# Kernel tuning notes

Hardware: AMD Instinct MI355X
Metric: run time of the kernel (lower is better)

The kernel has to match this reference:

```python
import jax, jax.numpy as jnp
import numpy as np
import math

T, B = 2048, 32
N_CLASSES = 64
D_MODEL = 512
N_LAYERS = 2
N_HEADS = 8
D_HEAD = 64
D_FF = N_HEADS * D_HEAD * 4  # 2048
E_VAL = (D_MODEL + 1) // 2   # 256 value-embedding dim
D_PE = D_MODEL // 2          # 256 positional dim (concatenated)
EPS_ATTN = 1e-6
EPS_LN = 1e-5


def _pe_table(t, d):
    pos = np.arange(t, dtype=np.float32)[:, None]
    div = np.exp(np.arange(0, d, 2, dtype=np.float32) * (-math.log(10000.0) / d))
    pe = np.zeros((t, d), dtype=np.float32)
    pe[:, 0::2] = np.sin(pos * div)
    pe[:, 1::2] = np.cos(pos * div)
    return jnp.asarray(pe)


def _ln(h, g, b):
    m = jnp.mean(h, axis=-1, keepdims=True)
    v = jnp.mean((h - m) ** 2, axis=-1, keepdims=True)
    return (h - m) * jax.lax.rsqrt(v + EPS_LN) * g + b


def setup_inputs() -> dict:
    key = jax.random.key(0)
    ks = jax.random.split(key, 12)
    s = 0.02
    L, dm, dff = N_LAYERS, D_MODEL, D_FF
    return {
        "x": jax.random.randint(ks[0], (T, B), 0, N_CLASSES),
        "E": jax.random.normal(ks[1], (N_CLASSES, E_VAL)) * s,
        "Wq": jax.random.normal(ks[2], (L, dm, dm)) * s, "bq": jnp.zeros((L, dm)),
        "Wk": jax.random.normal(ks[3], (L, dm, dm)) * s, "bk": jnp.zeros((L, dm)),
        "Wv": jax.random.normal(ks[4], (L, dm, dm)) * s, "bv": jnp.zeros((L, dm)),
        "Wo": jax.random.normal(ks[5], (L, dm, dm)) * s, "bo": jnp.zeros((L, dm)),
        "g1": jnp.ones((L, dm)), "be1": jnp.zeros((L, dm)),
        "W1": jax.random.normal(ks[6], (L, dm, dff)) * s, "b1": jnp.zeros((L, dff)),
        "W2": jax.random.normal(ks[7], (L, dff, dm)) * s, "b2": jnp.zeros((L, dm)),
        "g2": jnp.ones((L, dm)), "be2": jnp.zeros((L, dm)),
        "Wp": jax.random.normal(ks[8], (dm, N_CLASSES)) * s, "bp": jnp.zeros((N_CLASSES,)),
    }


def reference(x, E, Wq, bq, Wk, bk, Wv, bv, Wo, bo, g1, be1, W1, b1, W2, b2, g2, be2, Wp, bp):
    # embed tokens: x [T,B] -> [T,B,E_VAL]; concat positional (broadcast over batch) -> [T,B,D_MODEL]
    emb = E[x]
    pe = _pe_table(T, D_PE)
    h0 = jnp.concatenate([emb, jnp.broadcast_to(pe[:, None, :], (T, B, D_PE))], axis=-1)

    Si0 = jnp.zeros((N_LAYERS, B, N_HEADS, D_HEAD, D_HEAD), h0.dtype)  # sum_t k \otimes v
    Zi0 = jnp.zeros((N_LAYERS, B, N_HEADS, D_HEAD), h0.dtype)          # sum_t k

    phi = lambda u: jax.nn.elu(u) + 1.0  # linear-attention feature map

    def step(carry, xt):
        Si, Zi = carry
        h = xt  # [B, D_MODEL]
        for l in range(N_LAYERS):
            q = phi((h @ Wq[l] + bq[l]).reshape(B, N_HEADS, D_HEAD))
            k = phi((h @ Wk[l] + bk[l]).reshape(B, N_HEADS, D_HEAD))
            v = (h @ Wv[l] + bv[l]).reshape(B, N_HEADS, D_HEAD)
            Sl = Si[l] + k[..., :, None] * v[..., None, :]   # [B,H,D,D]
            Zl = Zi[l] + k
            num = jnp.einsum("bhd,bhdm->bhm", q, Sl)
            den = jnp.einsum("bhd,bhd->bh", q, Zl) + EPS_ATTN
            attn = (num / den[..., None]).reshape(B, N_HEADS * D_HEAD) @ Wo[l] + bo[l]
            h = _ln(h + attn, g1[l], be1[l])
            ff = jax.nn.relu(h @ W1[l] + b1[l]) @ W2[l] + b2[l]
            h = _ln(h + ff, g2[l], be2[l])
            Si = Si.at[l].set(Sl)
            Zi = Zi.at[l].set(Zl)
        return (Si, Zi), h

    _, ys = jax.lax.scan(step, (Si0, Zi0), h0)       # [T,B,D_MODEL]
    y_hat = jnp.transpose(ys, (1, 0, 2)) @ Wp + bp   # [B,T,N_CLASSES]
    return y_hat
```

## Files before the change

kernel.cpp:

```cpp
#include <hip/hip_runtime.h>


typedef unsigned short u16;
typedef __bf16 bf16x8 __attribute__((ext_vector_type(8)));
typedef float f32x4 __attribute__((ext_vector_type(4)));
typedef float f32x16 __attribute__((ext_vector_type(16)));

#define T_SEQ 2048
#define BATCH 32
#define NHEADS 8
#define CT 64
#define NCHUNK 32

#define SKEW(r, k) ((((k) + (((r) >> 3) << 3))) & 63)

__device__ __forceinline__ float b2f(u16 u) {
    union { unsigned int i; float f; } v; v.i = ((unsigned int)u) << 16; return v.f;
}
__device__ __forceinline__ u16 f2b(float f) {
    union { __bf16 b; u16 u; } v; v.b = (__bf16)f; return v.u;
}

__device__ __forceinline__ void gl_lds16(const u16* g, u16* l) {
    __builtin_amdgcn_global_load_lds(
        (const __attribute__((address_space(1))) void*)g,
        (__attribute__((address_space(3))) void*)l,
        16, 0, 0);
}

template<int ACT, bool RES>
__global__ __launch_bounds__(256) void gemm_mx(
    const u16* __restrict__ A, const u16* __restrict__ BT,
    const float* __restrict__ bias, const u16* __restrict__ R,
    u16* __restrict__ C,
    int M, int N, int K, int act_split, int nbn, int GM)
{
    __shared__ __align__(16) u16 As[128 * 64];
    __shared__ __align__(16) u16 Bs[128 * 64];

    const int bid = blockIdx.x;
    const int gsz = GM * nbn;
    const int grp = bid / gsz, rm = bid % gsz;
    const int bm = (grp * GM + rm % GM) * 128;
    const int bn = (rm / GM) * 128;

    const int tid = threadIdx.x;
    const int lane = tid & 63;
    const int w = tid >> 6;
    const int l32 = lane & 31;
    const int kh  = lane >> 5;
    const int wrow = (w >> 1) * 64, wcol = (w & 1) * 64;
    const int sr = lane >> 3;
    const int sg = lane & 7;

    f32x16 acc[2][2] = {};

    for (int k0 = 0; k0 < K; k0 += 64) {
        #pragma unroll
        for (int ch4 = 0; ch4 < 4; ch4++) {
            const int chunk = w * 4 + ch4;
            const int r = chunk * 8 + sr;
            const int gs = sg ^ (r & 7);
            gl_lds16(A  + (size_t)(bm + r) * K + k0 + gs * 8, As + chunk * 512);
            gl_lds16(BT + (size_t)(bn + r) * K + k0 + gs * 8, Bs + chunk * 512);
        }
        __syncthreads();
        #pragma unroll
        for (int step = 0; step < 4; step++) {
            const int gA = step * 2 + kh;
            bf16x8 af[2], bfv[2];
            #pragma unroll
            for (int i = 0; i < 2; i++) {
                const int r = wrow + i * 32 + l32;
                const int gq = gA ^ (r & 7);
                af[i] = *(const bf16x8*)&As[r * 64 + gq * 8];
            }
            #pragma unroll
            for (int j = 0; j < 2; j++) {
                const int r = wcol + j * 32 + l32;
                const int gq = gA ^ (r & 7);
                bfv[j] = *(const bf16x8*)&Bs[r * 64 + gq * 8];
            }
            #pragma unroll
            for (int i = 0; i < 2; i++)
                #pragma unroll
                for (int j = 0; j < 2; j++)
                    acc[i][j] = __builtin_amdgcn_mfma_f32_32x32x16_bf16(
                        af[i], bfv[j], acc[i][j], 0, 0, 0);
        }
        __syncthreads();
    }

    #pragma unroll
    for (int i = 0; i < 2; i++) {
        const int row0 = bm + wrow + i * 32 + 4 * kh;
        #pragma unroll
        for (int j = 0; j < 2; j++) {
            const int col = bn + wcol + j * 32 + l32;
            const float bb = bias[col];
            const bool phi = (ACT == 2) && (col < act_split);
            #pragma unroll
            for (int reg = 0; reg < 16; reg++) {
                const int m = row0 + (reg & 3) + 8 * (reg >> 2);
                float v = acc[i][j][reg] + bb;
                if (RES) v += b2f(R[(size_t)m * N + col]);
                if (ACT == 1) v = fmaxf(v, 0.f);
                if (ACT == 2) { if (phi) v = (v > 0.f) ? (v + 1.f) : __expf(v); }
                C[(size_t)m * N + col] = f2b(v);
            }
        }
    }
}

template<int BM, int BN, int WM, int WN>
__global__ __launch_bounds__(WM*WN*64) void gemm_sm(
    const u16* __restrict__ A, const u16* __restrict__ BT,
    const float* __restrict__ bias, float* __restrict__ C,
    int M, int N, int K)
{
    constexpr int BK = 32;
    constexpr int LDT = BK + 8;
    constexpr int NTHR = WM * WN * 64;
    __shared__ __align__(16) u16 As[BM * LDT];
    __shared__ __align__(16) u16 Bs[BN * LDT];

    const int tid = threadIdx.x;
    const int bm = blockIdx.y * BM;
    const int bn = blockIdx.x * BN;
    const int lane = tid & 63;
    const int wid = tid >> 6;
    const int wrow = (wid / WN) * (BM / WM);
    const int wcol = (wid % WN) * (BN / WN);
    constexpr int FM = BM / WM / 16;
    constexpr int FN = BN / WN / 16;
    const int lrow = lane & 15;
    const int lk = (lane >> 4) * 8;

    f32x4 acc[FM][FN] = {};

    for (int k0 = 0; k0 < K; k0 += BK) {
        #pragma unroll
        for (int g0 = 0; g0 < BM * 4; g0 += NTHR) {
            int g = g0 + tid;
            int row = g >> 2, kk = (g & 3) * 8;
            *(uint4*)&As[row * LDT + kk] =
                *(const uint4*)&A[(size_t)(bm + row) * K + k0 + kk];
        }
        #pragma unroll
        for (int g0 = 0; g0 < BN * 4; g0 += NTHR) {
            int g = g0 + tid;
            int row = g >> 2, kk = (g & 3) * 8;
            *(uint4*)&Bs[row * LDT + kk] =
                *(const uint4*)&BT[(size_t)(bn + row) * K + k0 + kk];
        }
        __syncthreads();
        bf16x8 af[FM], bfv[FN];
        #pragma unroll
        for (int i = 0; i < FM; i++)
            af[i] = *(const bf16x8*)&As[(wrow + i * 16 + lrow) * LDT + lk];
        #pragma unroll
        for (int j = 0; j < FN; j++)
            bfv[j] = *(const bf16x8*)&Bs[(wcol + j * 16 + lrow) * LDT + lk];
        #pragma unroll
        for (int i = 0; i < FM; i++)
            #pragma unroll
            for (int j = 0; j < FN; j++)
                acc[i][j] = __builtin_amdgcn_mfma_f32_16x16x32_bf16(
                    bfv[j], af[i], acc[i][j], 0, 0, 0);
        __syncthreads();
    }

    #pragma unroll
    for (int i = 0; i < FM; i++) {
        const int row = bm + wrow + i * 16 + lrow;
        #pragma unroll
        for (int j = 0; j < FN; j++) {
            const int col0 = bn + wcol + j * 16 + (lane >> 4) * 4;
            const float4 bb = *(const float4*)&bias[col0];
            float4 o = { acc[i][j][0] + bb.x, acc[i][j][1] + bb.y,
                         acc[i][j][2] + bb.z, acc[i][j][3] + bb.w };
            *(float4*)&C[(size_t)row * N + col0] = o;
        }
    }
}

__global__ __launch_bounds__(256) void prep_kernel(
    const float* __restrict__ Wq, const float* __restrict__ Wk,
    const float* __restrict__ Wv, const float* __restrict__ Wo,
    const float* __restrict__ W1, const float* __restrict__ W2,
    const float* __restrict__ Wp,
    const float* __restrict__ bq, const float* __restrict__ bk,
    const float* __restrict__ bv,
    u16* __restrict__ qkvT, u16* __restrict__ woT, u16* __restrict__ w1T,
    u16* __restrict__ w2T, u16* __restrict__ wpT, u16* __restrict__ pe,
    float* __restrict__ bqkv)
{
    __shared__ float tile[32][33];
    const int bid = blockIdx.x;
    const float* src; u16* dst; int K, N, bx, by;

    if (bid < 1536) {
        int l = bid / 768, r = bid % 768, m = r >> 8, t = r & 255;
        const float* s3[3] = { Wq, Wk, Wv };
        src = s3[m] + (size_t)l * 262144;
        dst = qkvT + (size_t)l * 786432 + (size_t)m * 262144;
        K = 512; N = 512; bx = t & 15; by = t >> 4;
    } else if (bid < 2048) {
        int r = bid - 1536, l = r >> 8, t = r & 255;
        src = Wo + (size_t)l * 262144; dst = woT + (size_t)l * 262144;
        K = 512; N = 512; bx = t & 15; by = t >> 4;
    } else if (bid < 4096) {
        int r = bid - 2048, l = r >> 10, t = r & 1023;
        src = W1 + (size_t)l * 1048576; dst = w1T + (size_t)l * 1048576;
        K = 512; N = 2048; bx = t & 63; by = t >> 6;
    } else if (bid < 6144) {
        int r = bid - 4096, l = r >> 10, t = r & 1023;
        src = W2 + (size_t)l * 1048576; dst = w2T + (size_t)l * 1048576;
        K = 2048; N = 512; bx = t & 15; by = t >> 4;
    } else if (bid < 6176) {
        int t = bid - 6144;
        src = Wp; dst = wpT; K = 512; N = 64; bx = t & 1; by = t >> 1;
    } else if (bid < 8224) {
        int id = (bid - 6176) * 256 + threadIdx.x;
        int t = id >> 8, j = id & 255;
        int i = j >> 1;
        float div = expf(-(float)(2 * i) * (9.210340371976184f / 256.f));
        float arg = (float)t * div;
        pe[id] = f2b((j & 1) ? cosf(arg) : sinf(arg));
        return;
    } else {
        int id = (bid - 8224) * 256 + threadIdx.x;
        if (id < 3072) {
            int l = id / 1536, i2 = id % 1536;
            float v = (i2 < 512) ? bq[l * 512 + i2]
                    : (i2 < 1024) ? bk[l * 512 + i2 - 512]
                                  : bv[l * 512 + i2 - 1024];
            bqkv[id] = v;
        }
        return;
    }

    int tx = threadIdx.x & 31, ty = threadIdx.x >> 5;
    #pragma unroll
    for (int yy = 0; yy < 4; yy++) {
        int k = by * 32 + ty + yy * 8;
        tile[ty + yy * 8][tx] = src[(size_t)k * N + bx * 32 + tx];
    }
    __syncthreads();
    #pragma unroll
    for (int yy = 0; yy < 4; yy++) {
        int n = bx * 32 + ty + yy * 8;
        dst[(size_t)n * K + by * 32 + tx] = f2b(tile[tx][ty + yy * 8]);
    }
}

__global__ __launch_bounds__(256) void embed_kernel(
    const int* __restrict__ x, const float* __restrict__ E,
    const u16* __restrict__ pe, u16* __restrict__ h, int b0)
{
    int idx = blockIdx.x * 256 + threadIdx.x;
    int e8 = idx * 8;
    int r = e8 >> 9;
    int c = e8 & 511;
    int t = r & (T_SEQ - 1);
    int b = b0 + (r >> 11);
    union { u16 u[8]; uint4 v; } o;
    if (c < 256) {
        const float* Ep = &E[(size_t)x[t * BATCH + b] * 256 + c];
        #pragma unroll
        for (int i = 0; i < 8; i++) o.u[i] = f2b(Ep[i]);
    } else {
        o.v = *(const uint4*)&pe[t * 256 + (c - 256)];
    }
    *(uint4*)&h[e8] = o.v;
}

__global__ __launch_bounds__(256) void attn_chunk_sums(
    const u16* __restrict__ qkv, u16* __restrict__ S, float* __restrict__ Z,
    int BHg)
{
    __shared__ __align__(16) u16 Kt[64 * 72], Vt[64 * 72];
    int bid = blockIdx.x;
    int bh = bid % BHg, c = bid / BHg;
    int bl = bh >> 3, hh = bh & 7;
    {
        const int m  = threadIdx.x & 7;
        const int d0 = m * 8;
        #pragma unroll
        for (int p = 0; p < 2; p++) {
            const int t = p * 32 + (threadIdx.x >> 3);
            size_t rr = ((size_t)(bl * T_SEQ + c * 64 + t)) * 1536 + hh * 64 + d0;
            uint4 kv = *(const uint4*)&qkv[rr + 512];
            uint4 vv = *(const uint4*)&qkv[rr + 1024];
            const u16* kp = (const u16*)&kv;
            const u16* vp = (const u16*)&vv;
            const int sk = (t + d0) & 63;
            u16* kb = &Kt[d0 * 72 + sk];
            u16* vb = &Vt[d0 * 72 + sk];
            #pragma unroll
            for (int s = 0; s < 8; s++) { kb[s * 72] = kp[s]; vb[s * 72] = vp[s]; }
        }
    }
    __syncthreads();
    int lane = threadIdx.x & 63;
    int w = threadIdx.x >> 6;
    int lrow = lane & 15, quad = lane >> 4;
    int m0 = w * 16;
    f32x4 acc[4] = {};
    #pragma unroll
    for (int k0 = 0; k0 < 64; k0 += 32) {
        const int ra = m0 + lrow;
        bf16x8 af = *(const bf16x8*)&Vt[ra * 72 + SKEW(ra, k0 + quad * 8)];
        #pragma unroll
        for (int jt = 0; jt < 4; jt++) {
            const int rb = jt * 16 + lrow;
            bf16x8 bf = *(const bf16x8*)&Kt[rb * 72 + SKEW(rb, k0 + quad * 8)];
            acc[jt] = __builtin_amdgcn_mfma_f32_16x16x32_bf16(bf, af, acc[jt], 0, 0, 0);
        }
    }
    size_t base = ((size_t)c * BHg + bh) * 4096;
    const int m = m0 + lrow;
    #pragma unroll
    for (int jt = 0; jt < 4; jt++) {
        const int d0 = jt * 16 + quad * 4;
        union { u16 q[4]; uint2 u; } pk;
        #pragma unroll
        for (int r = 0; r < 4; r++) pk.q[r] = f2b(acc[jt][r]);
        *(uint2*)&S[base + m * 64 + d0] = pk.u;
    }
    if (threadIdx.x < 64) {
        const int d = threadIdx.x;
        float z = 0.f;
        #pragma unroll
        for (int t8 = 0; t8 < 64; t8 += 8) {
            bf16x8 kk = *(const bf16x8*)&Kt[d * 72 + SKEW(d, t8)];
            #pragma unroll
            for (int u = 0; u < 8; u++) z += (float)kk[u];
        }
        Z[((size_t)c * BHg + bh) * 64 + d] = z;
    }
}

__global__ __launch_bounds__(256) void attn_prefix(
    u16* __restrict__ S, float* __restrict__ Z, int BHg)
{
    int gid = blockIdx.x * 256 + threadIdx.x;
    int bh = gid >> 12, e = gid & 4095;
    size_t stride = (size_t)BHg * 4096;
    size_t base = (size_t)bh * 4096 + e;
    float v[NCHUNK];
    #pragma unroll
    for (int c = 0; c < NCHUNK; c++) v[c] = b2f(S[base + c * stride]);
    float run = 0.f;
    #pragma unroll
    for (int c = 0; c < NCHUNK; c++) {
        float t = v[c]; S[base + c * stride] = f2b(run); run += t;
    }
    if (gid < BHg * 64) {
        size_t zb = (size_t)gid;
        size_t zs = (size_t)BHg * 64;
        float zv[NCHUNK];
        #pragma unroll
        for (int c = 0; c < NCHUNK; c++) zv[c] = Z[zb + c * zs];
        float zr = 0.f;
        #pragma unroll
        for (int c = 0; c < NCHUNK; c++) {
            float t = zv[c]; Z[zb + c * zs] = zr; zr += t;
        }
    }
}

__global__ __launch_bounds__(256) void attn_intra(
    const u16* __restrict__ qkv, const u16* __restrict__ Sp,
    const float* __restrict__ Zp, u16* __restrict__ out, int BHg)
{
    __shared__ __align__(16) u16 Qs[64 * 72], Ks[64 * 72], Vt[64 * 72],
                                 Ssh[64 * 72];
    __shared__ float Zsh[64], den2sh[64], den1sh[64];
    u16* Ps = Ks;
    int bid = blockIdx.x;
    int bh = bid % BHg, c = bid / BHg;
    int bl = bh >> 3, hh = bh & 7;
    size_t sbase = ((size_t)c * BHg + bh) * 4096;
    {
        const int m  = threadIdx.x & 7;
        const int d0 = m * 8;
        #pragma unroll
        for (int p = 0; p < 2; p++) {
            const int t = p * 32 + (threadIdx.x >> 3);
            size_t rr = ((size_t)(bl * T_SEQ + c * 64 + t)) * 1536 + hh * 64 + d0;
            *(uint4*)&Qs[t * 72 + d0]  = *(const uint4*)&qkv[rr];
            *(uint4*)&Ks[t * 72 + d0]  = *(const uint4*)&qkv[rr + 512];
            *(uint4*)&Ssh[t * 72 + d0] = *(const uint4*)&Sp[sbase + t * 64 + d0];
            uint4 vv = *(const uint4*)&qkv[rr + 1024];
            const u16* vp = (const u16*)&vv;
            const int sk = (t + d0) & 63;
            u16* vb = &Vt[d0 * 72 + sk];
            #pragma unroll
            for (int s = 0; s < 8; s++) vb[s * 72] = vp[s];
        }
    }
    if (threadIdx.x < 64)
        Zsh[threadIdx.x] = Zp[((size_t)c * BHg + bh) * 64 + threadIdx.x];
    __syncthreads();

    if (threadIdx.x < 64) {
        float s = 0.f;
        #pragma unroll
        for (int d8 = 0; d8 < 64; d8 += 8) {
            bf16x8 qq = *(const bf16x8*)&Qs[threadIdx.x * 72 + d8];
            #pragma unroll
            for (int u = 0; u < 8; u++) s += (float)qq[u] * Zsh[d8 + u];
        }
        den2sh[threadIdx.x] = s;
    }

    int lane = threadIdx.x & 63;
    int w = threadIdx.x >> 6;
    int lrow = lane & 15, quad = lane >> 4;
    int i0 = w * 16;

    f32x4 accp[4] = {};
    #pragma unroll
    for (int k0 = 0; k0 < 64; k0 += 32) {
        bf16x8 af = *(const bf16x8*)&Qs[(i0 + lrow) * 72 + k0 + quad * 8];
        #pragma unroll
        for (int jt = 0; jt < 4; jt++) {
            bf16x8 bf = *(const bf16x8*)&Ks[(jt * 16 + lrow) * 72 + k0 + quad * 8];
            accp[jt] = __builtin_amdgcn_mfma_f32_16x16x32_bf16(af, bf, accp[jt], 0, 0, 0);
        }
    }
    __syncthreads();
    #pragma unroll
    for (int r = 0; r < 4; r++) {
        int row = i0 + quad * 4 + r;
        float d1 = 0.f;
        #pragma unroll
        for (int jt = 0; jt < 4; jt++) {
            int col = jt * 16 + lrow;
            float pv = (col <= row) ? accp[jt][r] : 0.f;
            d1 += pv;
            Ps[row * 72 + col] = f2b(pv);
        }
        #pragma unroll
        for (int off = 1; off < 16; off <<= 1)
            d1 += __shfl_xor(d1, off, 64);
        if (lrow == 0) den1sh[row] = d1;
    }
    __syncthreads();

    f32x4 acco[4] = {};
    #pragma unroll
    for (int k0 = 0; k0 < 64; k0 += 32) {
        bf16x8 ps = *(const bf16x8*)&Ps[(i0 + lrow) * 72 + k0 + quad * 8];
        #pragma unroll
        for (int jt = 0; jt < 4; jt++) {
            const int rv = jt * 16 + lrow;
            bf16x8 vf = *(const bf16x8*)&Vt[rv * 72 + SKEW(rv, k0 + quad * 8)];
            acco[jt] = __builtin_amdgcn_mfma_f32_16x16x32_bf16(vf, ps, acco[jt], 0, 0, 0);
        }
    }
    #pragma unroll
    for (int k0 = 0; k0 < 64; k0 += 32) {
        bf16x8 qf = *(const bf16x8*)&Qs[(i0 + lrow) * 72 + k0 + quad * 8];
        #pragma unroll
        for (int jt = 0; jt < 4; jt++) {
            bf16x8 sf = *(const bf16x8*)&Ssh[(jt * 16 + lrow) * 72 + k0 + quad * 8];
            acco[jt] = __builtin_amdgcn_mfma_f32_16x16x32_bf16(sf, qf, acco[jt], 0, 0, 0);
        }
    }
    const int i = i0 + lrow;
    const float inv = 1.f / (den1sh[i] + den2sh[i] + 1e-6f);
    size_t orow = ((size_t)(bl * T_SEQ + c * 64 + i)) * 512 + hh * 64;
    #pragma unroll
    for (int jt = 0; jt < 4; jt++) {
        const int m0 = jt * 16 + quad * 4;
        union { u16 q[4]; uint2 u; } pk;
        #pragma unroll
        for (int r = 0; r < 4; r++) pk.q[r] = f2b(acco[jt][r] * inv);
        *(uint2*)&out[orow + m0] = pk.u;
    }
}

__global__ __launch_bounds__(256) void ln_kernel(
    const u16* __restrict__ s_in,
    const float* __restrict__ g, const float* __restrict__ be, u16* __restrict__ out)
{
    int row = blockIdx.x * 4 + (threadIdx.x >> 6);
    int lane = threadIdx.x & 63;
    size_t base = (size_t)row * 512 + lane * 8;
    uint4 hv = *(const uint4*)&s_in[base];
    const u16* hp = (const u16*)&hv;
    float x[8]; float s = 0.f;
    #pragma unroll
    for (int i = 0; i < 8; i++) { x[i] = b2f(hp[i]); s += x[i]; }
    #pragma unroll
    for (int off = 32; off > 0; off >>= 1) s += __shfl_xor(s, off, 64);
    float m = s * (1.f / 512.f);
    float vs = 0.f;
    #pragma unroll
    for (int i = 0; i < 8; i++) { float t = x[i] - m; vs += t * t; }
    #pragma unroll
    for (int off = 32; off > 0; off >>= 1) vs += __shfl_xor(vs, off, 64);
    float rstd = rsqrtf(vs * (1.f / 512.f) + 1e-5f);
    union { u16 u[8]; uint4 v; } o;
    #pragma unroll
    for (int i = 0; i < 8; i++)
        o.u[i] = f2b((x[i] - m) * rstd * g[lane * 8 + i] + be[lane * 8 + i]);
    *(uint4*)&out[base] = o.v;
}

extern "C" void kernel_launch(void* const* d_in, const int* in_sizes, int n_in,
                              void* d_out, int out_size, void* d_ws, size_t ws_size,
                              hipStream_t stream)
{
    const int*   x  = (const int*)d_in[0];
    const float* E  = (const float*)d_in[1];
    const float* Wq = (const float*)d_in[2];
    const float* bq = (const float*)d_in[3];
    const float* Wk = (const float*)d_in[4];
    const float* bk = (const float*)d_in[5];
    const float* Wv = (const float*)d_in[6];
    const float* bv = (const float*)d_in[7];
    const float* Wo = (const float*)d_in[8];
    const float* bo = (const float*)d_in[9];
    const float* g1 = (const float*)d_in[10];
    const float* be1= (const float*)d_in[11];
    const float* W1 = (const float*)d_in[12];
    const float* b1 = (const float*)d_in[13];
    const float* W2 = (const float*)d_in[14];
    const float* b2 = (const float*)d_in[15];
    const float* g2 = (const float*)d_in[16];
    const float* be2= (const float*)d_in[17];
    const float* Wp = (const float*)d_in[18];
    const float* bp = (const float*)d_in[19];

    char* p = (char*)d_ws;
    u16* qkvT = (u16*)p; p += (size_t)2 * 1536 * 512 * 2;
    u16* woT  = (u16*)p; p += (size_t)2 * 512 * 512 * 2;
    u16* w1T  = (u16*)p; p += (size_t)2 * 2048 * 512 * 2;
    u16* w2T  = (u16*)p; p += (size_t)2 * 512 * 2048 * 2;
    u16* wpT  = (u16*)p; p += (size_t)64 * 512 * 2;
    u16* pe   = (u16*)p; p += (size_t)T_SEQ * 256 * 2;
    float* bqkv = (float*)p; p += (size_t)16384;
    size_t fixed = (size_t)(p - (char*)d_ws);

    const size_t perB = 12648448ULL;
    int Bg = 32;
    while (Bg > 1 && fixed + (size_t)Bg * perB > ws_size) Bg >>= 1;
    const int rows = Bg * T_SEQ;
    const int BHg = Bg * NHEADS;
    const int nbm = rows / 128;

    u16* h      = (u16*)p; p += (size_t)rows * 512 * 2;
    u16* qkvBig = (u16*)p; p += (size_t)rows * 2048 * 2;
    u16* am     = (u16*)p; p += (size_t)rows * 512 * 2;
    float* Z    = (float*)p; p += (size_t)BHg * NCHUNK * 64 * 4;
    u16* qkv = qkvBig;
    u16* Sb  = qkvBig + (size_t)rows * 1536;
    u16* ff1 = qkvBig;
    u16* o_  = qkvBig;

    dim3 blk(256);

    prep_kernel<<<8236, blk, 0, stream>>>(
        Wq, Wk, Wv, Wo, W1, W2, Wp, bq, bk, bv,
        qkvT, woT, w1T, w2T, wpT, pe, bqkv);

    for (int b0 = 0; b0 < BATCH; b0 += Bg) {
        embed_kernel<<<rows / 4, blk, 0, stream>>>(x, E, pe, h, b0);

        for (int l = 0; l < 2; l++) {
            gemm_mx<2, false><<<dim3(nbm * 12), blk, 0, stream>>>(
                h, qkvT + (size_t)l * 786432, bqkv + l * 1536, nullptr, qkv,
                rows, 1536, 512, 1024, 12, 8);
            attn_chunk_sums<<<NCHUNK * BHg, blk, 0, stream>>>(qkv, Sb, Z, BHg);
            attn_prefix<<<BHg * 16, blk, 0, stream>>>(Sb, Z, BHg);
            attn_intra<<<NCHUNK * BHg, blk, 0, stream>>>(qkv, Sb, Z, am, BHg);
            gemm_mx<0, true><<<dim3(nbm * 4), blk, 0, stream>>>(
                am, woT + (size_t)l * 262144, bo + l * 512, h, o_,
                rows, 512, 512, 0, 4, 8);
            ln_kernel<<<rows / 4, blk, 0, stream>>>(o_, g1 + l * 512, be1 + l * 512, h);
            gemm_mx<1, false><<<dim3(nbm * 16), blk, 0, stream>>>(
                h, w1T + (size_t)l * 1048576, b1 + l * 2048, nullptr, ff1,
                rows, 2048, 512, 0, 16, 8);
            gemm_mx<0, true><<<dim3(nbm * 4), blk, 0, stream>>>(
                ff1, w2T + (size_t)l * 1048576, b2 + l * 512, h, am,
                rows, 512, 2048, 0, 4, 8);
            ln_kernel<<<rows / 4, blk, 0, stream>>>(am, g2 + l * 512, be2 + l * 512, h);
        }

        gemm_sm<64, 64, 2, 2><<<dim3(1, rows / 64), blk, 0, stream>>>(
            h, wpT, bp, (float*)d_out + (size_t)b0 * T_SEQ * 64, rows, 64, 512);
    }

    (void)in_sizes; (void)n_in; (void)out_size; (void)ws_size;
}
```

Measured before the change: 1.567 ms.

## Replace GEMM with 256x256 double-buffered 8-wave pipelined MFMA kernel

Replaces the 128x128 single-buffered GEMM with a 256x256 tile kernel using 8 waves, two LDS buffers, and prefetch of tile t+2 interleaved between four MFMA phases with barriers and setprio. It also remaps block IDs across XCDs (bid&7 striding) and changes grid sizes to match. The aim is to hide global-to-LDS latency behind MFMA work and raise operand reuse per tile. In exchange it uses 128KB of LDS per block and fewer blocks, which may hurt occupancy and tail balance on the smaller N=512 GEMMs.

```diff
diff --git a/kernel.cpp b/kernel.cpp
--- a/kernel.cpp
+++ b/kernel.cpp
@@ -29,74 +29,162 @@
 }
 
 template<int ACT, bool RES>
-__global__ __launch_bounds__(256) void gemm_mx(
+__global__ __launch_bounds__(512, 2) void gemm_p8(
     const u16* __restrict__ A, const u16* __restrict__ BT,
     const float* __restrict__ bias, const u16* __restrict__ R,
     u16* __restrict__ C,
-    int M, int N, int K, int act_split, int nbn, int GM)
-{
-    __shared__ __align__(16) u16 As[128 * 64];
-    __shared__ __align__(16) u16 Bs[128 * 64];
-
-    const int bid = blockIdx.x;
-    const int gsz = GM * nbn;
-    const int grp = bid / gsz, rm = bid % gsz;
-    const int bm = (grp * GM + rm % GM) * 128;
-    const int bn = (rm / GM) * 128;
+    int M, int N, int K, int act_split, int nbm)
+{
+    __shared__ __align__(16) u16 AsS[2][256 * 64];
+    __shared__ __align__(16) u16 BsS[2][256 * 64];
+
+    const int nwg = gridDim.x;
+    int bid = blockIdx.x;
+    const int q8 = nwg >> 3;
+    bid = (bid & 7) * q8 + (bid >> 3);
+    const int bm = (bid % nbm) * 256;
+    const int bn = (bid / nbm) * 256;
+    if (bm >= M || bn >= N) return;
 
     const int tid = threadIdx.x;
     const int lane = tid & 63;
-    const int w = tid >> 6;
+    const int w  = tid >> 6;
+    const int wr = w >> 2;
+    const int wc = w & 3;
     const int l32 = lane & 31;
     const int kh  = lane >> 5;
-    const int wrow = (w >> 1) * 64, wcol = (w & 1) * 64;
     const int sr = lane >> 3;
     const int sg = lane & 7;
 
-    f32x16 acc[2][2] = {};
-
-    for (int k0 = 0; k0 < K; k0 += 64) {
-        #pragma unroll
-        for (int ch4 = 0; ch4 < 4; ch4++) {
-            const int chunk = w * 4 + ch4;
-            const int r = chunk * 8 + sr;
-            const int gs = sg ^ (r & 7);
-            gl_lds16(A  + (size_t)(bm + r) * K + k0 + gs * 8, As + chunk * 512);
-            gl_lds16(BT + (size_t)(bn + r) * K + k0 + gs * 8, Bs + chunk * 512);
-        }
-        __syncthreads();
-        #pragma unroll
-        for (int step = 0; step < 4; step++) {
-            const int gA = step * 2 + kh;
-            bf16x8 af[2], bfv[2];
-            #pragma unroll
-            for (int i = 0; i < 2; i++) {
-                const int r = wrow + i * 32 + l32;
-                const int gq = gA ^ (r & 7);
-                af[i] = *(const bf16x8*)&As[r * 64 + gq * 8];
+    const int NT = K >> 6;
+
+    f32x16 acc[4][2] = {};
+
+    auto stage64 = [&](u16* lds, const u16* g, int rowbase, int k0, int row0) {
+        const int r = row0 + w * 8 + sr;
+        const int gs = sg ^ (r & 7);
+        gl_lds16(g + (size_t)(rowbase + r) * K + k0 + gs * 8,
+                 lds + (row0 + w * 8) * 64);
+    };
+
+    #pragma unroll
+    for (int qq = 0; qq < 4; qq++) stage64(AsS[0], A, bm, 0, qq * 64);
+    #pragma unroll
+    for (int qq = 0; qq < 4; qq++) stage64(BsS[0], BT, bn, 0, qq * 64);
+    #pragma unroll
+    for (int qq = 0; qq < 4; qq++) stage64(AsS[1], A, bm, 64, qq * 64);
+    #pragma unroll
+    for (int qq = 0; qq < 4; qq++) stage64(BsS[1], BT, bn, 64, qq * 64);
+    asm volatile("s_waitcnt vmcnt(8)" ::: "memory");
+    __builtin_amdgcn_s_barrier();
+
+    bf16x8 af[2][4], b0[4], b1[4];
+
+    for (int t = 0; t < NT; ++t) {
+        u16* As_ = AsS[t & 1];
+        u16* Bs_ = BsS[t & 1];
+        const int k2 = (t + 2) << 6;
+        const bool pf = (t + 2) < NT;
+
+        #pragma unroll
+        for (int mf = 0; mf < 2; mf++) {
+            const int r = wr * 128 + mf * 32 + l32;
+            #pragma unroll
+            for (int ks = 0; ks < 4; ks++) {
+                const int gq = (ks * 2 + kh) ^ (r & 7);
+                af[mf][ks] = *(const bf16x8*)&As_[r * 64 + gq * 8];
             }
-            #pragma unroll
-            for (int j = 0; j < 2; j++) {
-                const int r = wcol + j * 32 + l32;
-                const int gq = gA ^ (r & 7);
-                bfv[j] = *(const bf16x8*)&Bs[r * 64 + gq * 8];
+        }
+        {
+            const int rb = wc * 64 + l32;
+            #pragma unroll
+            for (int ks = 0; ks < 4; ks++) {
+                const int gq = (ks * 2 + kh) ^ (rb & 7);
+                b0[ks] = *(const bf16x8*)&Bs_[rb * 64 + gq * 8];
             }
-            #pragma unroll
-            for (int i = 0; i < 2; i++)
-                #pragma unroll
-                for (int j = 0; j < 2; j++)
-                    acc[i][j] = __builtin_amdgcn_mfma_f32_32x32x16_bf16(
-                        af[i], bfv[j], acc[i][j], 0, 0, 0);
-        }
-        __syncthreads();
-    }
-
-    #pragma unroll
-    for (int i = 0; i < 2; i++) {
-        const int row0 = bm + wrow + i * 32 + 4 * kh;
+        }
+        __builtin_amdgcn_s_barrier();
+        asm volatile("s_waitcnt lgkmcnt(0)" ::: "memory");
+        __builtin_amdgcn_sched_barrier(0);
+        __builtin_amdgcn_s_setprio(1);
+        #pragma unroll
+        for (int ks = 0; ks < 4; ks++)
+            #pragma unroll
+            for (int mf = 0; mf < 2; mf++)
+                acc[mf][0] = __builtin_amdgcn_mfma_f32_32x32x16_bf16(
+                    af[mf][ks], b0[ks], acc[mf][0], 0, 0, 0);
+        __builtin_amdgcn_s_setprio(0);
+        __builtin_amdgcn_s_barrier();
+
+        {
+            const int rb = wc * 64 + 32 + l32;
+            #pragma unroll
+            for (int ks = 0; ks < 4; ks++) {
+                const int gq = (ks * 2 + kh) ^ (rb & 7);
+                b1[ks] = *(const bf16x8*)&Bs_[rb * 64 + gq * 8];
+            }
+        }
+        if (pf) { stage64(As_, A, bm, k2, 0); stage64(As_, A, bm, k2, 128); }
+        __builtin_amdgcn_s_barrier();
+        asm volatile("s_waitcnt lgkmcnt(0)" ::: "memory");
+        __builtin_amdgcn_sched_barrier(0);
+        __builtin_amdgcn_s_setprio(1);
+        #pragma unroll
+        for (int ks = 0; ks < 4; ks++)
+            #pragma unroll
+            for (int mf = 0; mf < 2; mf++)
+                acc[mf][1] = __builtin_amdgcn_mfma_f32_32x32x16_bf16(
+                    af[mf][ks], b1[ks], acc[mf][1], 0, 0, 0);
+        __builtin_amdgcn_s_setprio(0);
+        __builtin_amdgcn_s_barrier();
+
+        #pragma unroll
+        for (int mf = 0; mf < 2; mf++) {
+            const int r = wr * 128 + 64 + mf * 32 + l32;
+            #pragma unroll
+            for (int ks = 0; ks < 4; ks++) {
+                const int gq = (ks * 2 + kh) ^ (r & 7);
+                af[mf][ks] = *(const bf16x8*)&As_[r * 64 + gq * 8];
+            }
+        }
+        if (pf) { stage64(Bs_, BT, bn, k2, 0); stage64(Bs_, BT, bn, k2, 64); }
+        __builtin_amdgcn_s_barrier();
+        asm volatile("s_waitcnt lgkmcnt(0)" ::: "memory");
+        __builtin_amdgcn_sched_barrier(0);
+        __builtin_amdgcn_s_setprio(1);
+        #pragma unroll
+        for (int ks = 0; ks < 4; ks++)
+            #pragma unroll
+            for (int mf = 0; mf < 2; mf++)
+                acc[2 + mf][0] = __builtin_amdgcn_mfma_f32_32x32x16_bf16(
+                    af[mf][ks], b0[ks], acc[2 + mf][0], 0, 0, 0);
+        __builtin_amdgcn_s_setprio(0);
+        __builtin_amdgcn_s_barrier();
+
+        if (pf) {
+            stage64(Bs_, BT, bn, k2, 128); stage64(Bs_, BT, bn, k2, 192);
+            stage64(As_, A,  bm, k2, 64);  stage64(As_, A,  bm, k2, 192);
+        }
+        __builtin_amdgcn_s_barrier();
+        __builtin_amdgcn_s_setprio(1);
+        #pragma unroll
+        for (int ks = 0; ks < 4; ks++)
+            #pragma unroll
+            for (int mf = 0; mf < 2; mf++)
+                acc[2 + mf][1] = __builtin_amdgcn_mfma_f32_32x32x16_bf16(
+                    af[mf][ks], b1[ks], acc[2 + mf][1], 0, 0, 0);
+        __builtin_amdgcn_s_setprio(0);
+        if (pf) asm volatile("s_waitcnt vmcnt(8)" ::: "memory");
+        else    asm volatile("s_waitcnt vmcnt(0)" ::: "memory");
+        __builtin_amdgcn_s_barrier();
+    }
+
+    #pragma unroll
+    for (int i = 0; i < 4; i++) {
+        const int row0 = bm + wr * 128 + i * 32 + 4 * kh;
         #pragma unroll
         for (int j = 0; j < 2; j++) {
-            const int col = bn + wcol + j * 32 + l32;
+            const int col = bn + wc * 64 + j * 32 + l32;
             const float bb = bias[col];
             const bool phi = (ACT == 2) && (col < act_split);
             #pragma unroll
@@ -550,7 +638,7 @@
     while (Bg > 1 && fixed + (size_t)Bg * perB > ws_size) Bg >>= 1;
     const int rows = Bg * T_SEQ;
     const int BHg = Bg * NHEADS;
-    const int nbm = rows / 128;
+    const int nbm = rows / 256;
 
     u16* h      = (u16*)p; p += (size_t)rows * 512 * 2;
     u16* qkvBig = (u16*)p; p += (size_t)rows * 2048 * 2;
@@ -562,6 +650,7 @@
     u16* o_  = qkvBig;
 
     dim3 blk(256);
+    dim3 blk8(512);
 
     prep_kernel<<<8236, blk, 0, stream>>>(
         Wq, Wk, Wv, Wo, W1, W2, Wp, bq, bk, bv,
@@ -571,22 +660,22 @@
         embed_kernel<<<rows / 4, blk, 0, stream>>>(x, E, pe, h, b0);
 
         for (int l = 0; l < 2; l++) {
-            gemm_mx<2, false><<<dim3(nbm * 12), blk, 0, stream>>>(
+            gemm_p8<2, false><<<dim3(nbm * 6), blk8, 0, stream>>>(
                 h, qkvT + (size_t)l * 786432, bqkv + l * 1536, nullptr, qkv,
-                rows, 1536, 512, 1024, 12, 8);
+                rows, 1536, 512, 1024, nbm);
             attn_chunk_sums<<<NCHUNK * BHg, blk, 0, stream>>>(qkv, Sb, Z, BHg);
             attn_prefix<<<BHg * 16, blk, 0, stream>>>(Sb, Z, BHg);
             attn_intra<<<NCHUNK * BHg, blk, 0, stream>>>(qkv, Sb, Z, am, BHg);
-            gemm_mx<0, true><<<dim3(nbm * 4), blk, 0, stream>>>(
+            gemm_p8<0, true><<<dim3(nbm * 2), blk8, 0, stream>>>(
                 am, woT + (size_t)l * 262144, bo + l * 512, h, o_,
-                rows, 512, 512, 0, 4, 8);
+                rows, 512, 512, 0, nbm);
             ln_kernel<<<rows / 4, blk, 0, stream>>>(o_, g1 + l * 512, be1 + l * 512, h);
-            gemm_mx<1, false><<<dim3(nbm * 16), blk, 0, stream>>>(
+            gemm_p8<1, false><<<dim3(nbm * 8), blk8, 0, stream>>>(
                 h, w1T + (size_t)l * 1048576, b1 + l * 2048, nullptr, ff1,
-                rows, 2048, 512, 0, 16, 8);
-            gemm_mx<0, true><<<dim3(nbm * 4), blk, 0, stream>>>(
+                rows, 2048, 512, 0, nbm);
+            gemm_p8<0, true><<<dim3(nbm * 2), blk8, 0, stream>>>(
                 ff1, w2T + (size_t)l * 1048576, b2 + l * 512, h, am,
-                rows, 512, 2048, 0, 4, 8);
+                rows, 512, 2048, 0, nbm);
             ln_kernel<<<rows / 4, blk, 0, stream>>>(am, g2 + l * 512, be2 + l * 512, h);
         }
 
```

After: 1.602 ms. 1.02x slower.
